# Kernel optimization log

Hardware: AMD Instinct MI355X
Metric: run time of the kernel (lower is better)

Reference implementation:

```python
import jax, jax.numpy as jnp
import numpy as np

jax.config.update("jax_enable_x64", True)

Q30 = 1 << 30


def multiply_M(x, M0):
    # gemmlowp SaturatingRoundingDoublingHighMul in int64: (x*M0 + nudge) >> 31
    ab = x * M0.astype(jnp.int64)
    nudge = jnp.where(ab >= 0, jnp.int64(Q30), jnp.int64(1 - Q30))
    return (ab + nudge) >> 31


def rounding_shift(cur, shift):
    # gemmlowp RoundingDivideByPOT; shift >= 0, broadcastable int64
    mask = (jnp.int64(1) << shift) - 1
    remainder = cur & mask
    threshold = (mask >> 1) + jnp.where(cur < 0, jnp.int64(1), jnp.int64(0))
    return ((cur >> shift) + jnp.where(remainder > threshold, jnp.int64(1), jnp.int64(0))).astype(jnp.int32)


def setup_inputs() -> dict:
    key = jax.random.key(0)
    ks = jax.random.split(key, 9)
    B, C, H, W = 32, 256, 56, 56
    NCL = 4
    # quantized activations (stored float, cast to int32 inside forward like torch's .type(IntTensor))
    x = jax.random.randint(ks[0], (B, C, H, W), 0, 256).astype(jnp.float32)
    weight = jax.random.randint(ks[1], (NCL, C), 0, 256, dtype=jnp.int32)
    bias = jax.random.randint(ks[2], (NCL, C), -1000, 1000, dtype=jnp.int32)
    z1 = jax.random.randint(ks[3], (NCL,), 0, 256, dtype=jnp.int32)
    z2 = jax.random.randint(ks[4], (NCL,), 0, 256, dtype=jnp.int32)
    z3 = jax.random.randint(ks[5], (NCL,), -128, 128, dtype=jnp.int32)
    M0 = jax.random.randint(ks[6], (NCL,), 1 << 30, 2147483647, dtype=jnp.int32)
    shift = jax.random.randint(ks[7], (NCL,), -2, 12, dtype=jnp.int32)
    batch_cluster = jax.random.randint(ks[8], (B,), 0, NCL, dtype=jnp.int32)
    return dict(x=x, weight=weight, bias=bias, z1=z1, z2=z2, z3=z3,
                M0=M0, shift=shift, batch_cluster=batch_cluster)


def reference(x, weight, bias, z1, z2, z3, M0, shift, batch_cluster):
    # _pcq path: per-sample cluster selection, int32 affine, fixed-point requantize
    bc = batch_cluster
    xi = x.astype(jnp.int32)                                   # [B,C,H,W]
    w = weight[bc][:, :, None, None]                           # [B,C,1,1] int32
    b = bias[bc][:, :, None, None]
    Z1 = z1[bc][:, None, None, None]
    Z2 = z2[bc][:, None, None, None]
    Z3 = z3[bc][:, None, None, None]
    m0 = M0[bc][:, None, None, None]
    sh = shift[bc].astype(jnp.int64)[:, None, None, None]
    # subsum computed in int32 (matches torch), then widened to int64
    subsum = (xi * w - xi * Z2 - w * Z1 + Z1 * Z2 + b).astype(jnp.int64)
    # negative shift -> pre-left-shift then M0-mul, round-shift by 0
    # positive shift -> M0-mul then round-shift by `shift` (per-sample, 4d)
    s_neg = jnp.maximum(-sh, jnp.int64(0))
    s_pos = jnp.maximum(sh, jnp.int64(0))
    multiplied = multiply_M(subsum << s_neg, m0)
    total = rounding_shift(multiplied, s_pos) + Z3
    total = jnp.clip(total, -128, 127)  # bit == 8
    return total.astype(jnp.float32)
```

## Files before the change

### kernel.cpp

```cpp
#include <hip/hip_runtime.h>


#define CCH 256
#define HW  3136
#define HW4 784

typedef float v4f __attribute__((ext_vector_type(4)));

__device__ __forceinline__ v4f proc4(v4f v, int A, int Bc, int s_neg,
                                     int s_pos, int m0, int mask, int half,
                                     int Z3) {
    v4f r;
    #pragma unroll
    for (int j = 0; j < 4; ++j) {
        int xi = (int)v[j];
        int sub = (xi * A + Bc) << s_neg;
        long long ab = (long long)sub * (long long)m0;
        long long nudge = ab >= 0 ? (1LL << 30) : (1LL - (1LL << 30));
        int mul = (int)((ab + nudge) >> 31);
        int rem = mul & mask;
        int thr = half + (mul < 0 ? 1 : 0);
        int tot = (mul >> s_pos) + (rem > thr ? 1 : 0) + Z3;
        tot = tot < -128 ? -128 : (tot > 127 ? 127 : tot);
        r[j] = (float)tot;
    }
    return r;
}

__global__ __launch_bounds__(256) void qbn_kernel(
    const float* __restrict__ x,
    const int*   __restrict__ weight,
    const int*   __restrict__ bias,
    const int*   __restrict__ z1,
    const int*   __restrict__ z2,
    const int*   __restrict__ z3,
    const int*   __restrict__ M0,
    const int*   __restrict__ shiftp,
    const int*   __restrict__ bcluster,
    float*       __restrict__ out)
{
    const int slice = blockIdx.x;
    const int b = slice >> 8;
    const int c = slice & 255;

    const int cl = bcluster[b];
    const int w  = weight[cl * CCH + c];
    const int bi = bias[cl * CCH + c];
    const int Z1 = z1[cl], Z2 = z2[cl], Z3 = z3[cl];
    const int m0 = M0[cl];
    const int sh = shiftp[cl];
    const int s_neg = sh < 0 ? -sh : 0;
    const int s_pos = sh > 0 ?  sh : 0;

    const int A    = w - Z2;
    const int Bc   = bi - w * Z1 + Z1 * Z2;
    const int mask = (1 << s_pos) - 1;
    const int half = mask >> 1;

    const v4f* xin  = reinterpret_cast<const v4f*>(x   + (size_t)slice * HW);
    v4f*       xout = reinterpret_cast<v4f*>      (out + (size_t)slice * HW);

    const int t = threadIdx.x;
    v4f v0 = xin[t];
    v4f v1 = xin[t + 256];
    v4f v2 = xin[t + 512];
    v4f vt;
    const bool tail = t < (HW4 - 768);
    if (tail) vt = xin[t + 768];

    v4f r0 = proc4(v0, A, Bc, s_neg, s_pos, m0, mask, half, Z3);
    v4f r1 = proc4(v1, A, Bc, s_neg, s_pos, m0, mask, half, Z3);
    v4f r2 = proc4(v2, A, Bc, s_neg, s_pos, m0, mask, half, Z3);

    __builtin_nontemporal_store(r0, &xout[t]);
    __builtin_nontemporal_store(r1, &xout[t + 256]);
    __builtin_nontemporal_store(r2, &xout[t + 512]);
    if (tail) {
        v4f rt = proc4(vt, A, Bc, s_neg, s_pos, m0, mask, half, Z3);
        __builtin_nontemporal_store(rt, &xout[t + 768]);
    }
}

extern "C" void kernel_launch(void* const* d_in, const int* in_sizes, int n_in,
                              void* d_out, int out_size, void* d_ws, size_t ws_size,
                              hipStream_t stream) {
    const float* x      = (const float*)d_in[0];
    const int*   weight = (const int*)  d_in[1];
    const int*   bias   = (const int*)  d_in[2];
    const int*   z1     = (const int*)  d_in[3];
    const int*   z2     = (const int*)  d_in[4];
    const int*   z3     = (const int*)  d_in[5];
    const int*   M0     = (const int*)  d_in[6];
    const int*   shiftp = (const int*)  d_in[7];
    const int*   bc     = (const int*)  d_in[8];
    float*       out    = (float*)d_out;

    const int B = in_sizes[8];
    const int nslices = B * CCH;
    hipLaunchKernelGGL(qbn_kernel, dim3(nslices), dim3(256), 0, stream,
                       x, weight, bias, z1, z2, z3, M0, shiftp, bc, out);
}
```

Before: 35.64 us.

## Process four channel slices per block with register double-buffered loads

Each block now handles four consecutive (batch, channel) slices instead of one, so the grid is four times smaller. It prefetches the next slice's input into registers while computing and storing the current one. The goal is to amortize per-block parameter loads and launch overhead and to keep more loads in flight per thread. In exchange, each thread uses more registers, which may lower occupancy, and with fewer blocks there is less parallelism for latency hiding across the GPU.

```diff
diff --git a/kernel.cpp b/kernel.cpp
--- a/kernel.cpp
+++ b/kernel.cpp
@@ -4,6 +4,7 @@
 #define CCH 256
 #define HW  3136
 #define HW4 784
+#define SPB 4
 
 typedef float v4f __attribute__((ext_vector_type(4)));
 
@@ -39,45 +40,60 @@
     const int*   __restrict__ bcluster,
     float*       __restrict__ out)
 {
-    const int slice = blockIdx.x;
-    const int b = slice >> 8;
-    const int c = slice & 255;
+    const int t = threadIdx.x;
+    const int slice0 = blockIdx.x * SPB;
+    const int b  = slice0 >> 8;
+    const int c0 = slice0 & 255;
 
     const int cl = bcluster[b];
-    const int w  = weight[cl * CCH + c];
-    const int bi = bias[cl * CCH + c];
     const int Z1 = z1[cl], Z2 = z2[cl], Z3 = z3[cl];
     const int m0 = M0[cl];
     const int sh = shiftp[cl];
     const int s_neg = sh < 0 ? -sh : 0;
     const int s_pos = sh > 0 ?  sh : 0;
+    const int mask  = (1 << s_pos) - 1;
+    const int half  = mask >> 1;
 
-    const int A    = w - Z2;
-    const int Bc   = bi - w * Z1 + Z1 * Z2;
-    const int mask = (1 << s_pos) - 1;
-    const int half = mask >> 1;
+    int A[SPB], Bc[SPB];
+    #pragma unroll
+    for (int s = 0; s < SPB; ++s) {
+        const int w = weight[cl * CCH + c0 + s];
+        A[s]  = w - Z2;
+        Bc[s] = bias[cl * CCH + c0 + s] - w * Z1 + Z1 * Z2;
+    }
 
-    const v4f* xin  = reinterpret_cast<const v4f*>(x   + (size_t)slice * HW);
-    v4f*       xout = reinterpret_cast<v4f*>      (out + (size_t)slice * HW);
+    const v4f* xin  = reinterpret_cast<const v4f*>(x   + (size_t)slice0 * HW);
+    v4f*       xout = reinterpret_cast<v4f*>      (out + (size_t)slice0 * HW);
+    const bool tail = t < (HW4 - 768);
 
-    const int t = threadIdx.x;
-    v4f v0 = xin[t];
-    v4f v1 = xin[t + 256];
-    v4f v2 = xin[t + 512];
-    v4f vt;
-    const bool tail = t < (HW4 - 768);
-    if (tail) vt = xin[t + 768];
+    v4f u0 = xin[t];
+    v4f u1 = xin[t + 256];
+    v4f u2 = xin[t + 512];
+    v4f ut = {0, 0, 0, 0};
+    if (tail) ut = xin[t + 768];
 
-    v4f r0 = proc4(v0, A, Bc, s_neg, s_pos, m0, mask, half, Z3);
-    v4f r1 = proc4(v1, A, Bc, s_neg, s_pos, m0, mask, half, Z3);
-    v4f r2 = proc4(v2, A, Bc, s_neg, s_pos, m0, mask, half, Z3);
-
-    __builtin_nontemporal_store(r0, &xout[t]);
-    __builtin_nontemporal_store(r1, &xout[t + 256]);
-    __builtin_nontemporal_store(r2, &xout[t + 512]);
-    if (tail) {
-        v4f rt = proc4(vt, A, Bc, s_neg, s_pos, m0, mask, half, Z3);
-        __builtin_nontemporal_store(rt, &xout[t + 768]);
+    #pragma unroll
+    for (int s = 0; s < SPB; ++s) {
+        v4f n0 = {0,0,0,0}, n1 = {0,0,0,0}, n2 = {0,0,0,0}, nt = {0,0,0,0};
+        if (s + 1 < SPB) {
+            const v4f* nin = xin + (size_t)(s + 1) * HW4;
+            n0 = nin[t];
+            n1 = nin[t + 256];
+            n2 = nin[t + 512];
+            if (tail) nt = nin[t + 768];
+        }
+        v4f r0 = proc4(u0, A[s], Bc[s], s_neg, s_pos, m0, mask, half, Z3);
+        v4f r1 = proc4(u1, A[s], Bc[s], s_neg, s_pos, m0, mask, half, Z3);
+        v4f r2 = proc4(u2, A[s], Bc[s], s_neg, s_pos, m0, mask, half, Z3);
+        v4f* o = xout + (size_t)s * HW4;
+        __builtin_nontemporal_store(r0, &o[t]);
+        __builtin_nontemporal_store(r1, &o[t + 256]);
+        __builtin_nontemporal_store(r2, &o[t + 512]);
+        if (tail) {
+            v4f rt = proc4(ut, A[s], Bc[s], s_neg, s_pos, m0, mask, half, Z3);
+            __builtin_nontemporal_store(rt, &o[t + 768]);
+        }
+        u0 = n0; u1 = n1; u2 = n2; ut = nt;
     }
 }
 
@@ -96,7 +112,7 @@
     float*       out    = (float*)d_out;
 
     const int B = in_sizes[8];
-    const int nslices = B * CCH;
-    hipLaunchKernelGGL(qbn_kernel, dim3(nslices), dim3(256), 0, stream,
+    const int nblocks = B * CCH / SPB;
+    hipLaunchKernelGGL(qbn_kernel, dim3(nblocks), dim3(256), 0, stream,
                        x, weight, bias, z1, z2, z3, M0, shiftp, bc, out);
 }
```

Measured after the change: 36.83 us. 3.3% more time.
